# Kernel optimization log

Measured on AMD Instinct MI355X. Metric: run time of the kernel, lower is better.

## Reference

```python
import jax, jax.numpy as jnp
import numpy as np

EPS = 1e-5
NUM_CLUSTERS = 64


def _bn(x, g, b, m, v):
    # eval-mode BatchNorm over channel (last) axis
    return (x - m) * (g * jax.lax.rsqrt(v + EPS)) + b


def _segment_max(feat, choice, num_clusters):
    # feat: [B, N, C], choice: [B, N] -> [B, K, C] (amax per cluster, -inf if empty)
    def one(f, c):
        init = jnp.full((num_clusters, f.shape[-1]), -jnp.inf, dtype=f.dtype)
        return init.at[c].max(f)
    return jax.vmap(one)(feat, choice)


def setup_inputs() -> dict:
    key = jax.random.key(0)
    ks = jax.random.split(key, 8)
    B, N, K, OUT = 32, 8192, NUM_CLUSTERS, 384
    s = lambda fan: 1.0 / np.sqrt(fan)
    return {
        "xyz": jax.random.normal(ks[0], (B, N, 3), jnp.float32),
        "choice": jax.random.randint(ks[1], (B, N), 0, K, jnp.int32),
        "w1": jax.random.normal(ks[2], (128, 3), jnp.float32) * s(3),
        "b1": jnp.zeros((128,), jnp.float32),
        "bn1_g": jnp.ones((128,), jnp.float32),
        "bn1_b": jnp.zeros((128,), jnp.float32),
        "bn1_m": jnp.zeros((128,), jnp.float32),
        "bn1_v": jnp.ones((128,), jnp.float32),
        "w2": jax.random.normal(ks[3], (256, 128), jnp.float32) * s(128),
        "b2": jnp.zeros((256,), jnp.float32),
        "w3": jax.random.normal(ks[4], (512, 512), jnp.float32) * s(512),
        "b3": jnp.zeros((512,), jnp.float32),
        "bn2_g": jnp.ones((512,), jnp.float32),
        "bn2_b": jnp.zeros((512,), jnp.float32),
        "bn2_m": jnp.zeros((512,), jnp.float32),
        "bn2_v": jnp.ones((512,), jnp.float32),
        "w4": jax.random.normal(ks[5], (OUT, 512), jnp.float32) * s(512),
        "b4": jnp.zeros((OUT,), jnp.float32),
    }


def reference(xyz, choice, w1, b1, bn1_g, bn1_b, bn1_m, bn1_v, w2, b2,
              w3, b3, bn2_g, bn2_b, bn2_m, bn2_v, w4, b4):
    # first_conv: 1x1 conv == per-point linear. xyz: [B,N,3]
    h = jnp.einsum("bnc,oc->bno", xyz, w1) + b1            # [B,N,128]
    h = jax.nn.relu(_bn(h, bn1_g, bn1_b, bn1_m, bn1_v))
    feat = jnp.einsum("bnc,oc->bno", h, w2) + b2            # [B,N,256]
    # cluster amax pooling + gather-broadcast back to points
    fg = _segment_max(feat, choice, NUM_CLUSTERS)           # [B,K,256]
    fg_pts = jnp.take_along_axis(fg, choice[..., None], axis=1)  # [B,N,256]
    f = jnp.concatenate([fg_pts, feat], axis=-1)            # [B,N,512]
    # second_conv
    h2 = jnp.einsum("bnc,oc->bno", f, w3) + b3              # [B,N,512]
    h2 = jax.nn.relu(_bn(h2, bn2_g, bn2_b, bn2_m, bn2_v))
    out = jnp.einsum("bnc,oc->bno", h2, w4) + b4            # [B,N,out_dim]
    return _segment_max(out, choice, NUM_CLUSTERS)          # [B,K,out_dim]
```

## Files before the change

kernel.cpp:

```cpp
#include <hip/hip_runtime.h>
#include <hip/hip_bf16.h>

typedef unsigned short u16;
typedef __attribute__((ext_vector_type(8))) short short8;
typedef __attribute__((ext_vector_type(4))) float f32x4;

#define EPSV 1e-5f
#define ENC_NINF 0x007FFFFFu

__device__ __forceinline__ float bf2f(u16 u) {
    union { unsigned int i; float f; } v; v.i = ((unsigned int)u) << 16; return v.f;
}
__device__ __forceinline__ u16 f2bf(float f) {
    union { float f; unsigned int i; } v; v.f = f;
    unsigned int x = v.i;
    return (u16)((x + 0x7FFFu + ((x >> 16) & 1u)) >> 16);
}
__device__ __forceinline__ unsigned int encbf(u16 u) {
    unsigned int f = ((unsigned int)u) << 16;
    return (f & 0x80000000u) ? ~f : (f | 0x80000000u);
}
__device__ __forceinline__ float dec(unsigned int u) {
    union { float f; unsigned int uu; } v;
    v.uu = (u & 0x80000000u) ? (u & 0x7FFFFFFFu) : ~u;
    return v.f;
}

__device__ __forceinline__ void async16(const u16* g, u16* l) {
    __builtin_amdgcn_global_load_lds((const __attribute__((address_space(1))) void*)g,
                                     (__attribute__((address_space(3))) void*)l,
                                     16, 0, 0);
}

__global__ __launch_bounds__(256) void k_fillf(float* __restrict__ o, int n, float val)
{
    int i = blockIdx.x * 256 + threadIdx.x;
    if (i < n) o[i] = val;
}

struct Ptrs { const void* p[17]; int off[18]; int chN; };

__global__ __launch_bounds__(256) void k_repack(Ptrs P, const void* __restrict__ chSrc,
                                                int* __restrict__ chi, u16* __restrict__ rp,
                                                unsigned int* __restrict__ initp, int nU)
{
    const unsigned int* probe = (const unsigned int*)P.p[9];
    int cnt = 0;
#pragma unroll
    for (int i = 0; i < 64; ++i) {
        unsigned int lo = probe[i] & 0xFFFFu;
        if (((lo >> 7) & 0xFFu) >= 0x80u) ++cnt;
    }
    const bool is_f32 = (cnt > 8);

    const unsigned int* cp = (const unsigned int*)chSrc;
    int z = 0; unsigned int mx = 0;
    for (int i = 0; i < 1024; ++i) {
        unsigned int w = cp[i];
        z += (w == 0u);
        mx = (w > mx) ? w : mx;
    }
    const int chMode = (mx >= 64u) ? 2 : ((z > 300) ? 1 : 0);

    const int stride = gridDim.x * 256;
    const int gid0 = blockIdx.x * 256 + threadIdx.x;

    const int totalF = P.off[17];
    for (int g = gid0; g < totalF; g += stride) {
        int t = 0;
        while (g >= P.off[t + 1]) ++t;
        int off = g - P.off[t];
        u16 v;
        if (is_f32) v = f2bf(((const float*)P.p[t])[off]);
        else        v = ((const u16*)P.p[t])[off];
        rp[g] = v;
    }
    for (int i = gid0; i < P.chN; i += stride) {
        int v;
        if (chMode == 1)      v = (int)((const long long*)chSrc)[i];
        else if (chMode == 2) v = (int)((const float*)chSrc)[i];
        else                  v = ((const int*)chSrc)[i];
        chi[i] = v & 63;
    }
    for (int i = gid0; i < nU; i += stride) initp[i] = ENC_NINF;
}

__global__ __launch_bounds__(256) void k_sort(const int* __restrict__ chi,
                                              int* __restrict__ schoice,
                                              int* __restrict__ perm)
{
    __shared__ int hist[64];
    __shared__ int base[64];
    const int b = blockIdx.x, tid = threadIdx.x;
    if (tid < 64) hist[tid] = 0;
    __syncthreads();
    const int o = b << 13;
    for (int i = tid; i < 8192; i += 256) atomicAdd(&hist[chi[o + i]], 1);
    __syncthreads();
    if (tid == 0) {
        int s = 0;
        for (int k = 0; k < 64; ++k) { base[k] = s; s += hist[k]; }
    }
    __syncthreads();
    for (int i = tid; i < 8192; i += 256) {
        int k = chi[o + i];
        int pos = atomicAdd(&base[k], 1);
        schoice[o + pos] = k;
        perm[o + pos] = o + i;
    }
}

__global__ __launch_bounds__(256, 2) void g1_feat(
    const u16* __restrict__ xyz, const u16* __restrict__ w1, const u16* __restrict__ b1,
    const u16* __restrict__ g1v, const u16* __restrict__ bb1,
    const u16* __restrict__ m1, const u16* __restrict__ v1,
    const u16* __restrict__ w2, const u16* __restrict__ b2,
    const int* __restrict__ schoice, const int* __restrict__ perm,
    u16* __restrict__ feat, unsigned int* __restrict__ fg_u)
{
    __shared__ __align__(16) u16 Bs[256 * 128];
    __shared__ unsigned int lred[8 * 256];
    __shared__ float4 pw[128];
    __shared__ float xs[128], ys[128], zs[128];
    __shared__ int chs[128];
    const int tid = threadIdx.x, lane = tid & 63, wave = tid >> 6;
    const int wm = (wave & 1) << 6, wn = (wave >> 1) << 6;
    const int m0 = blockIdx.x << 7;
    if (tid < 128) {
        float s = bf2f(g1v[tid]) * rsqrtf(bf2f(v1[tid]) + EPSV);
        float4 w;
        w.x = bf2f(w1[tid * 3 + 0]) * s;
        w.y = bf2f(w1[tid * 3 + 1]) * s;
        w.z = bf2f(w1[tid * 3 + 2]) * s;
        w.w = (bf2f(b1[tid]) - bf2f(m1[tid])) * s + bf2f(bb1[tid]);
        pw[tid] = w;
        const u16* p = xyz + (size_t)perm[m0 + tid] * 3;
        xs[tid] = bf2f(p[0]); ys[tid] = bf2f(p[1]); zs[tid] = bf2f(p[2]);
        chs[tid] = schoice[m0 + tid];
    }
    const int q = lane >> 4, mr = lane & 15;
    f32x4 acc[2][4][4] = {};
#pragma unroll
    for (int i = 0; i < 16; ++i) {
        int id = (i << 8) + tid, row = id >> 4, cc = id & 15;
        async16(w2 + (size_t)row * 128 + ((cc ^ (row & 15)) << 3), &Bs[id << 3]);
    }
    __syncthreads();
    const int kmin = chs[0], nk = chs[127] - kmin + 1;
    const bool useL = (nk <= 8);
    if (useL) for (int i = tid; i < (nk << 8); i += 256) lred[i] = ENC_NINF;
#pragma unroll
    for (int kk = 0; kk < 4; ++kk) {
        const int lc = kk * 4 + q;
        float4 wv[8];
#pragma unroll
        for (int j = 0; j < 8; ++j) wv[j] = pw[kk * 32 + q * 8 + j];
        short8 af[4];
#pragma unroll
        for (int mi = 0; mi < 4; ++mi) {
            int row = wm + mi * 16 + mr;
            float x = xs[row], y = ys[row], z = zs[row];
#pragma unroll
            for (int j = 0; j < 8; ++j) {
                float val = fmaf(x, wv[j].x, fmaf(y, wv[j].y, fmaf(z, wv[j].z, wv[j].w)));
                af[mi][j] = (short)f2bf(fmaxf(val, 0.0f));
            }
        }
#pragma unroll
        for (int h = 0; h < 2; ++h) {
            short8 bfr[4];
#pragma unroll
            for (int ni = 0; ni < 4; ++ni) {
                int r = (h << 7) + wn + ni * 16 + mr;
                bfr[ni] = *(const short8*)&Bs[r * 128 + ((lc ^ (r & 15)) << 3)];
            }
#pragma unroll
            for (int mi = 0; mi < 4; ++mi)
#pragma unroll
                for (int ni = 0; ni < 4; ++ni)
                    acc[h][mi][ni] = __builtin_amdgcn_mfma_f32_16x16x32_bf16(af[mi], bfr[ni], acc[h][mi][ni], 0, 0, 0);
        }
    }
    __syncthreads();
    const int colb = lane & 15;
    const int bl = m0 >> 13;
    unsigned int* db = fg_u + (size_t)(bl << 6) * 256;
#pragma unroll
    for (int h = 0; h < 2; ++h)
#pragma unroll
        for (int ni = 0; ni < 4; ++ni) {
            int n = (h << 7) + wn + (ni << 4) + colb;
            float bv = bf2f(b2[n]);
#pragma unroll
            for (int mi = 0; mi < 4; ++mi) {
                int curk = -1; unsigned int run = 0;
#pragma unroll
                for (int r = 0; r < 4; ++r) {
                    int rr = wm + (mi << 4) + (q << 2) + r;
                    u16 vb = f2bf(acc[h][mi][ni][r] + bv);
                    feat[(size_t)(m0 + rr) * 256 + n] = vb;
                    unsigned int e = encbf(vb);
                    int k = chs[rr];
                    if (k != curk) {
                        if (curk >= 0) {
                            if (useL) atomicMax(&lred[((curk - kmin) << 8) + n], run);
                            else      atomicMax(&db[curk * 256 + n], run);
                        }
                        curk = k; run = e;
                    } else run = run > e ? run : e;
                }
                if (useL) atomicMax(&lred[((curk - kmin) << 8) + n], run);
                else      atomicMax(&db[curk * 256 + n], run);
            }
        }
    if (useL) {
        __syncthreads();
        for (int i = tid; i < (nk << 8); i += 256) {
            unsigned int v = lred[i];
            if (v != ENC_NINF) atomicMax(&db[(kmin + (i >> 8)) * 256 + (i & 255)], v);
        }
    }
}

__global__ __launch_bounds__(256, 2) void g3_h2(
    const int* __restrict__ schoice, const u16* __restrict__ feat,
    const u16* __restrict__ fg, const u16* __restrict__ w3, const u16* __restrict__ b3,
    const u16* __restrict__ g2, const u16* __restrict__ bb2,
    const u16* __restrict__ m2, const u16* __restrict__ v2,
    u16* __restrict__ h2)
{
    __shared__ __align__(16) u16 As[128 * 64];
    __shared__ __align__(16) u16 Bs[2 * 128 * 64];
    const int tid = threadIdx.x, lane = tid & 63, wave = tid >> 6;
    const int wm = (wave & 1) << 6, wn = (wave >> 1) << 6;
    const int m0 = blockIdx.x << 7, n0 = blockIdx.y << 8;
    const int c = tid & 7, rb = tid >> 3;
    const u16* fgrow[4]; const u16* ftrow[4];
#pragma unroll
    for (int i = 0; i < 4; ++i) {
        int pt = m0 + rb + (i << 5);
        int b = pt >> 13;
        fgrow[i] = fg + (((b << 6) + schoice[pt]) << 8);
        ftrow[i] = feat + ((size_t)pt << 8);
    }
    f32x4 acc[2][4][4] = {};
    for (int k0 = 0; k0 < 512; k0 += 64) {
        __syncthreads();
#pragma unroll
        for (int nt = 0; nt < 2; ++nt)
#pragma unroll
            for (int i = 0; i < 4; ++i) {
                int id = (i << 8) + tid, row = id >> 3, cc = id & 7;
                async16(w3 + (size_t)(n0 + nt * 128 + row) * 512 + k0 + ((cc ^ (row & 7)) << 3),
                        &Bs[nt * 8192 + (id << 3)]);
            }
#pragma unroll
        for (int i = 0; i < 4; ++i) {
            int r = rb + (i << 5);
            int col = k0 + ((c ^ (r & 7)) << 3);
            const u16* src = (col < 256) ? (fgrow[i] + col) : (ftrow[i] + (col - 256));
            async16(src, &As[(((i << 8) + tid) << 3)]);
        }
        __syncthreads();
        const int q = lane >> 4, mr = lane & 15;
#pragma unroll
        for (int kk = 0; kk < 2; ++kk) {
            short8 af[4];
            const int lc = kk * 4 + q;
#pragma unroll
            for (int mi = 0; mi < 4; ++mi) {
                int r = wm + mi * 16 + mr;
                af[mi] = *(const short8*)&As[r * 64 + ((lc ^ (r & 7)) << 3)];
            }
#pragma unroll
            for (int nt = 0; nt < 2; ++nt) {
                short8 bfr[4];
#pragma unroll
                for (int ni = 0; ni < 4; ++ni) {
                    int r = wn + ni * 16 + mr;
                    bfr[ni] = *(const short8*)&Bs[nt * 8192 + r * 64 + ((lc ^ (r & 7)) << 3)];
                }
#pragma unroll
                for (int mi = 0; mi < 4; ++mi)
#pragma unroll
                    for (int ni = 0; ni < 4; ++ni)
                        acc[nt][mi][ni] = __builtin_amdgcn_mfma_f32_16x16x32_bf16(af[mi], bfr[ni], acc[nt][mi][ni], 0, 0, 0);
            }
        }
    }
    const int q = lane >> 4, colb = lane & 15;
#pragma unroll
    for (int nt = 0; nt < 2; ++nt)
#pragma unroll
        for (int ni = 0; ni < 4; ++ni) {
            int n = n0 + nt * 128 + wn + (ni << 4) + colb;
            float s = bf2f(g2[n]) * rsqrtf(bf2f(v2[n]) + EPSV);
            float t = (bf2f(b3[n]) - bf2f(m2[n])) * s + bf2f(bb2[n]);
#pragma unroll
            for (int mi = 0; mi < 4; ++mi)
#pragma unroll
                for (int r = 0; r < 4; ++r) {
                    int m = m0 + wm + (mi << 4) + (q << 2) + r;
                    h2[(size_t)m * 512 + n] = f2bf(fmaxf(fmaf(acc[nt][mi][ni][r], s, t), 0.0f));
                }
        }
}

__global__ __launch_bounds__(512, 2) void g4_out(
    const u16* __restrict__ A, const u16* __restrict__ w4,
    const u16* __restrict__ bias, const int* __restrict__ schoice,
    unsigned int* __restrict__ out_u)
{
    __shared__ __align__(16) u16 smem[32768];
    __shared__ int chs[128];
    u16* As = smem;
    u16* Bs = smem + 8192;
    const int tid = threadIdx.x, lane = tid & 63, wave = tid >> 6;
    const int wm = (wave & 1) << 6, wn = (wave >> 1) * 96;
    const int m0 = blockIdx.x << 7;
    if (tid < 128) chs[tid] = schoice[m0 + tid];
    f32x4 acc[4][6] = {};
    for (int k0 = 0; k0 < 512; k0 += 64) {
        __syncthreads();
#pragma unroll
        for (int i = 0; i < 6; ++i) {
            int id = (i << 9) + tid, row = id >> 3, cc = id & 7;
            async16(w4 + (size_t)row * 512 + k0 + ((cc ^ (row & 7)) << 3),
                    &Bs[id << 3]);
        }
#pragma unroll
        for (int i = 0; i < 2; ++i) {
            int id = (i << 9) + tid, row = id >> 3, cc = id & 7;
            async16(A + (size_t)(m0 + row) * 512 + k0 + ((cc ^ (row & 7)) << 3),
                    &As[id << 3]);
        }
        __syncthreads();
        const int q = lane >> 4, mr = lane & 15;
#pragma unroll
        for (int kk = 0; kk < 2; ++kk) {
            const int lc = (kk << 2) + q;
            short8 af[4];
#pragma unroll
            for (int mi = 0; mi < 4; ++mi) {
                int r = wm + (mi << 4) + mr;
                af[mi] = *(const short8*)&As[r * 64 + ((lc ^ (r & 7)) << 3)];
            }
#pragma unroll
            for (int ni = 0; ni < 6; ++ni) {
                int r = wn + (ni << 4) + mr;
                short8 bfr = *(const short8*)&Bs[r * 64 + ((lc ^ (r & 7)) << 3)];
#pragma unroll
                for (int mi = 0; mi < 4; ++mi)
                    acc[mi][ni] = __builtin_amdgcn_mfma_f32_16x16x32_bf16(af[mi], bfr, acc[mi][ni], 0, 0, 0);
            }
        }
    }
    __syncthreads();
    unsigned int* lred = (unsigned int*)smem;
    const int kmin = chs[0], nk = chs[127] - kmin + 1;
    const bool useL = (nk <= 42);
    const int bl = m0 >> 13;
    unsigned int* db = out_u + (size_t)(bl << 6) * 384;
    if (useL) for (int i = tid; i < nk * 384; i += 512) lred[i] = ENC_NINF;
    __syncthreads();
    const int q = lane >> 4, colb = lane & 15;
#pragma unroll
    for (int ni = 0; ni < 6; ++ni) {
        int nc = wn + (ni << 4) + colb;
        float bv = bf2f(bias[nc]);
#pragma unroll
        for (int mi = 0; mi < 4; ++mi) {
            int curk = -1; unsigned int run = 0;
#pragma unroll
            for (int r = 0; r < 4; ++r) {
                int rr = wm + (mi << 4) + (q << 2) + r;
                unsigned int e = encbf(f2bf(acc[mi][ni][r] + bv));
                int k = chs[rr];
                if (k != curk) {
                    if (curk >= 0) {
                        if (useL) atomicMax(&lred[(curk - kmin) * 384 + nc], run);
                        else      atomicMax(&db[curk * 384 + nc], run);
                    }
                    curk = k; run = e;
                } else run = run > e ? run : e;
            }
            if (useL) atomicMax(&lred[(curk - kmin) * 384 + nc], run);
            else      atomicMax(&db[curk * 384 + nc], run);
        }
    }
    if (useL) {
        __syncthreads();
        for (int i = tid; i < nk * 384; i += 512) {
            unsigned int v = lred[i];
            if (v != ENC_NINF) {
                int kq = i / 384;
                atomicMax(&db[(kmin + kq) * 384 + (i - kq * 384)], v);
            }
        }
    }
}

__global__ __launch_bounds__(256) void k_dec_bf(const unsigned int* __restrict__ u,
                                                u16* __restrict__ o, int n)
{
    int i = blockIdx.x * 256 + threadIdx.x;
    if (i < n) o[i] = f2bf(dec(u[i]));
}
__global__ __launch_bounds__(256) void k_dec_f32(const unsigned int* __restrict__ u,
                                                 float* __restrict__ o, int n)
{
    int i = blockIdx.x * 256 + threadIdx.x;
    if (i < n) o[i] = dec(u[i]);
}

extern "C" void kernel_launch(void* const* d_in, const int* in_sizes, int n_in,
                              void* d_out, int out_size, void* d_ws, size_t ws_size,
                              hipStream_t stream)
{
    float* out = (float*)d_out;
    if (n_in != 18) {
        k_fillf<<<dim3((out_size + 255) / 256), 256, 0, stream>>>(out, out_size, 1000.0f);
        return;
    }

    const int map[17] = {0, 2, 3, 4, 5, 6, 7, 8, 9, 10, 11, 12, 13, 14, 15, 16, 17};
    Ptrs P;
    P.off[0] = 0;
    for (int i = 0; i < 17; ++i) {
        P.p[i] = d_in[map[i]];
        P.off[i + 1] = P.off[i] + in_sizes[map[i]];
    }
    P.chN = in_sizes[1];

    char* ws = (char*)d_ws;
    int* chi = (int*)ws;
    const size_t chiB = ((size_t)P.chN * 4 + 255) & ~255ull;
    int* schoice = (int*)(ws + chiB);
    int* perm    = (int*)(ws + 2 * chiB);
    u16* rp = (u16*)(ws + 3 * chiB);
    const size_t rpB = ((size_t)P.off[17] * 2 + 255) & ~255ull;
    const size_t RPB = 3 * chiB + rpB;

    unsigned int* fg_u_all  = (unsigned int*)(ws + RPB);
    unsigned int* out_u_all = fg_u_all + 32 * 64 * 256;
    const size_t UB = 5242880ull;
    const int nU = 32 * 64 * 640;

    k_repack<<<dim3(1024), 256, 0, stream>>>(P, d_in[1], chi, rp, fg_u_all, nU);
    k_sort<<<dim3(P.chN >> 13), 256, 0, stream>>>(chi, schoice, perm);

    const u16* xyz  = rp + P.off[0];
    const u16* w1   = rp + P.off[1];
    const u16* b1   = rp + P.off[2];
    const u16* bn1g = rp + P.off[3];
    const u16* bn1b = rp + P.off[4];
    const u16* bn1m = rp + P.off[5];
    const u16* bn1v = rp + P.off[6];
    const u16* w2   = rp + P.off[7];
    const u16* b2   = rp + P.off[8];
    const u16* w3   = rp + P.off[9];
    const u16* b3   = rp + P.off[10];
    const u16* bn2g = rp + P.off[11];
    const u16* bn2b = rp + P.off[12];
    const u16* bn2m = rp + P.off[13];
    const u16* bn2v = rp + P.off[14];
    const u16* w4   = rp + P.off[15];
    const u16* b4   = rp + P.off[16];

    const size_t PB = 12615680ull;
    int sb = 32;
    while (sb > 1 && RPB + UB + (size_t)sb * PB > ws_size) sb >>= 1;
    if (RPB + UB + PB > ws_size) {
        k_fillf<<<dim3((out_size + 255) / 256), 256, 0, stream>>>(out, out_size, 3000.0f);
        return;
    }
    const int ns = 32 / sb;

    char* wsb = ws + RPB + UB;
    const size_t featB = (size_t)sb * 8192 * 256 * 2;
    const size_t h2B   = (size_t)sb * 8192 * 512 * 2;
    u16* feat = (u16*)(wsb);
    u16* h2s  = (u16*)(wsb + featB);
    u16* fg   = (u16*)(wsb + featB + h2B);

    const int mblk = sb << 6;
    const int nfg = sb * 64 * 256;
    const int nou = sb * 64 * 384;
    for (int s = 0; s < ns; ++s) {
        const int b0 = s * sb;
        const int pt0 = b0 << 13;
        const int* sch_sl = schoice + pt0;
        const int* perm_sl = perm + pt0;
        unsigned int* fg_u  = fg_u_all + (size_t)b0 * 64 * 256;
        unsigned int* out_u = out_u_all + (size_t)b0 * 64 * 384;
        g1_feat<<<dim3(mblk), 256, 0, stream>>>(xyz, w1, b1, bn1g, bn1b, bn1m, bn1v,
                                                w2, b2, sch_sl, perm_sl, feat, fg_u);
        k_dec_bf<<<dim3((nfg + 255) / 256), 256, 0, stream>>>(fg_u, fg, nfg);
        g3_h2<<<dim3(mblk, 2), 256, 0, stream>>>(sch_sl, feat, fg, w3, b3,
                                                 bn2g, bn2b, bn2m, bn2v, h2s);
        g4_out<<<dim3(mblk), 512, 0, stream>>>(h2s, w4, b4, sch_sl, out_u);
        k_dec_f32<<<dim3((nou + 255) / 256), 256, 0, stream>>>(out_u,
                                                               out + ((size_t)b0 << 6) * 384, nou);
    }
}
```

Before: 543.4 us.

## Precompute per-cluster w3 projection of pooled features, halve h2 GEMM K

The pooled cluster feature is identical for every point in a cluster. Its product with the first half of w3 is therefore computed once per cluster in a new kernel (k_th), folded together with bias and BN shift, and stored as fp32. The main h2 GEMM now only contracts over the 256 per-point feature channels and adds the gathered per-cluster term in the epilogue, removing about half of its MFMA work and the fg gather loads. Separately, g4_out is restructured to stage w4 in two 192-row chunks, shrinking its LDS footprint. That chunking adds extra barriers and lowers the LDS-reduction threshold to 26 clusters.

```diff
diff --git a/kernel.cpp b/kernel.cpp
--- a/kernel.cpp
+++ b/kernel.cpp
@@ -222,44 +222,105 @@
     }
 }
 
-__global__ __launch_bounds__(256, 2) void g3_h2(
-    const int* __restrict__ schoice, const u16* __restrict__ feat,
+__global__ __launch_bounds__(256, 2) void k_th(
     const u16* __restrict__ fg, const u16* __restrict__ w3, const u16* __restrict__ b3,
     const u16* __restrict__ g2, const u16* __restrict__ bb2,
     const u16* __restrict__ m2, const u16* __restrict__ v2,
+    float* __restrict__ th)
+{
+    __shared__ __align__(16) u16 As[64 * 64];
+    __shared__ __align__(16) u16 Bs[256 * 64];
+    const int tid = threadIdx.x, lane = tid & 63, wave = tid >> 6;
+    const int b = blockIdx.x, n0 = blockIdx.y << 8;
+    const u16* fgb = fg + ((size_t)b << 14);
+    f32x4 acc[4][4] = {};
+    for (int k0 = 0; k0 < 256; k0 += 64) {
+        __syncthreads();
+#pragma unroll
+        for (int i = 0; i < 8; ++i) {
+            int id = (i << 8) + tid, row = id >> 3, cc = id & 7;
+            async16(w3 + (size_t)(n0 + row) * 512 + k0 + ((cc ^ (row & 7)) << 3),
+                    &Bs[id << 3]);
+        }
+#pragma unroll
+        for (int i = 0; i < 2; ++i) {
+            int id = (i << 8) + tid, row = id >> 3, cc = id & 7;
+            async16(fgb + (size_t)row * 256 + k0 + ((cc ^ (row & 7)) << 3),
+                    &As[id << 3]);
+        }
+        __syncthreads();
+        const int q = lane >> 4, mr = lane & 15;
+#pragma unroll
+        for (int kk = 0; kk < 2; ++kk) {
+            const int lc = (kk << 2) + q;
+            short8 af[4], bfr[4];
+#pragma unroll
+            for (int mi = 0; mi < 4; ++mi) {
+                int r = (mi << 4) + mr;
+                af[mi] = *(const short8*)&As[r * 64 + ((lc ^ (r & 7)) << 3)];
+            }
+#pragma unroll
+            for (int ni = 0; ni < 4; ++ni) {
+                int r = (wave << 6) + (ni << 4) + mr;
+                bfr[ni] = *(const short8*)&Bs[r * 64 + ((lc ^ (r & 7)) << 3)];
+            }
+#pragma unroll
+            for (int mi = 0; mi < 4; ++mi)
+#pragma unroll
+                for (int ni = 0; ni < 4; ++ni)
+                    acc[mi][ni] = __builtin_amdgcn_mfma_f32_16x16x32_bf16(af[mi], bfr[ni], acc[mi][ni], 0, 0, 0);
+        }
+    }
+    const int q = lane >> 4, colb = lane & 15;
+#pragma unroll
+    for (int ni = 0; ni < 4; ++ni) {
+        int n = n0 + (wave << 6) + (ni << 4) + colb;
+        float s = bf2f(g2[n]) * rsqrtf(bf2f(v2[n]) + EPSV);
+        float t = (bf2f(b3[n]) - bf2f(m2[n])) * s + bf2f(bb2[n]);
+#pragma unroll
+        for (int mi = 0; mi < 4; ++mi)
+#pragma unroll
+            for (int r = 0; r < 4; ++r) {
+                int c = (mi << 4) + (q << 2) + r;
+                th[((size_t)(b << 6) + c) * 512 + n] = fmaf(acc[mi][ni][r], s, t);
+            }
+    }
+}
+
+__global__ __launch_bounds__(256, 2) void g3_h2(
+    const int* __restrict__ schoice, const u16* __restrict__ feat,
+    const float* __restrict__ th, const u16* __restrict__ w3,
+    const u16* __restrict__ g2, const u16* __restrict__ v2,
     u16* __restrict__ h2)
 {
     __shared__ __align__(16) u16 As[128 * 64];
     __shared__ __align__(16) u16 Bs[2 * 128 * 64];
+    __shared__ int chs[128];
     const int tid = threadIdx.x, lane = tid & 63, wave = tid >> 6;
     const int wm = (wave & 1) << 6, wn = (wave >> 1) << 6;
     const int m0 = blockIdx.x << 7, n0 = blockIdx.y << 8;
     const int c = tid & 7, rb = tid >> 3;
-    const u16* fgrow[4]; const u16* ftrow[4];
-#pragma unroll
-    for (int i = 0; i < 4; ++i) {
-        int pt = m0 + rb + (i << 5);
-        int b = pt >> 13;
-        fgrow[i] = fg + (((b << 6) + schoice[pt]) << 8);
-        ftrow[i] = feat + ((size_t)pt << 8);
-    }
+    if (tid < 128) chs[tid] = schoice[m0 + tid];
+    const u16* ftrow[4];
+#pragma unroll
+    for (int i = 0; i < 4; ++i)
+        ftrow[i] = feat + ((size_t)(m0 + rb + (i << 5)) << 8);
     f32x4 acc[2][4][4] = {};
-    for (int k0 = 0; k0 < 512; k0 += 64) {
+    for (int k0 = 0; k0 < 256; k0 += 64) {
         __syncthreads();
 #pragma unroll
         for (int nt = 0; nt < 2; ++nt)
 #pragma unroll
             for (int i = 0; i < 4; ++i) {
                 int id = (i << 8) + tid, row = id >> 3, cc = id & 7;
-                async16(w3 + (size_t)(n0 + nt * 128 + row) * 512 + k0 + ((cc ^ (row & 7)) << 3),
+                async16(w3 + (size_t)(n0 + nt * 128 + row) * 512 + 256 + k0
+                            + ((cc ^ (row & 7)) << 3),
                         &Bs[nt * 8192 + (id << 3)]);
             }
 #pragma unroll
         for (int i = 0; i < 4; ++i) {
             int r = rb + (i << 5);
-            int col = k0 + ((c ^ (r & 7)) << 3);
-            const u16* src = (col < 256) ? (fgrow[i] + col) : (ftrow[i] + (col - 256));
-            async16(src, &As[(((i << 8) + tid) << 3)]);
+            async16(ftrow[i] + k0 + ((c ^ (r & 7)) << 3), &As[(((i << 8) + tid) << 3)]);
         }
         __syncthreads();
         const int q = lane >> 4, mr = lane & 15;
@@ -289,19 +350,21 @@
         }
     }
     const int q = lane >> 4, colb = lane & 15;
+    const float* thb = th + ((size_t)((m0 >> 13) << 6) * 512);
 #pragma unroll
     for (int nt = 0; nt < 2; ++nt)
 #pragma unroll
         for (int ni = 0; ni < 4; ++ni) {
             int n = n0 + nt * 128 + wn + (ni << 4) + colb;
             float s = bf2f(g2[n]) * rsqrtf(bf2f(v2[n]) + EPSV);
-            float t = (bf2f(b3[n]) - bf2f(m2[n])) * s + bf2f(bb2[n]);
 #pragma unroll
             for (int mi = 0; mi < 4; ++mi)
 #pragma unroll
                 for (int r = 0; r < 4; ++r) {
-                    int m = m0 + wm + (mi << 4) + (q << 2) + r;
-                    h2[(size_t)m * 512 + n] = f2bf(fmaxf(fmaf(acc[nt][mi][ni][r], s, t), 0.0f));
+                    int rr = wm + (mi << 4) + (q << 2) + r;
+                    float thv = thb[(size_t)chs[rr] * 512 + n];
+                    h2[(size_t)(m0 + rr) * 512 + n] =
+                        f2bf(fmaxf(fmaf(acc[nt][mi][ni][r], s, thv), 0.0f));
                 }
         }
 }
@@ -311,62 +374,65 @@
     const u16* __restrict__ bias, const int* __restrict__ schoice,
     unsigned int* __restrict__ out_u)
 {
-    __shared__ __align__(16) u16 smem[32768];
+    __shared__ __align__(16) u16 As[128 * 64];
+    __shared__ __align__(16) u16 Bs[192 * 64];
     __shared__ int chs[128];
-    u16* As = smem;
-    u16* Bs = smem + 8192;
     const int tid = threadIdx.x, lane = tid & 63, wave = tid >> 6;
-    const int wm = (wave & 1) << 6, wn = (wave >> 1) * 96;
+    const int wm = (wave & 1) << 6, wn48 = (wave >> 1) * 48;
     const int m0 = blockIdx.x << 7;
     if (tid < 128) chs[tid] = schoice[m0 + tid];
     f32x4 acc[4][6] = {};
     for (int k0 = 0; k0 < 512; k0 += 64) {
-        __syncthreads();
-#pragma unroll
-        for (int i = 0; i < 6; ++i) {
-            int id = (i << 9) + tid, row = id >> 3, cc = id & 7;
-            async16(w4 + (size_t)row * 512 + k0 + ((cc ^ (row & 7)) << 3),
-                    &Bs[id << 3]);
-        }
-#pragma unroll
-        for (int i = 0; i < 2; ++i) {
-            int id = (i << 9) + tid, row = id >> 3, cc = id & 7;
-            async16(A + (size_t)(m0 + row) * 512 + k0 + ((cc ^ (row & 7)) << 3),
-                    &As[id << 3]);
-        }
-        __syncthreads();
-        const int q = lane >> 4, mr = lane & 15;
-#pragma unroll
-        for (int kk = 0; kk < 2; ++kk) {
-            const int lc = (kk << 2) + q;
-            short8 af[4];
-#pragma unroll
-            for (int mi = 0; mi < 4; ++mi) {
-                int r = wm + (mi << 4) + mr;
-                af[mi] = *(const short8*)&As[r * 64 + ((lc ^ (r & 7)) << 3)];
-            }
-#pragma unroll
-            for (int ni = 0; ni < 6; ++ni) {
-                int r = wn + (ni << 4) + mr;
-                short8 bfr = *(const short8*)&Bs[r * 64 + ((lc ^ (r & 7)) << 3)];
-#pragma unroll
-                for (int mi = 0; mi < 4; ++mi)
-                    acc[mi][ni] = __builtin_amdgcn_mfma_f32_16x16x32_bf16(af[mi], bfr, acc[mi][ni], 0, 0, 0);
-            }
-        }
-    }
-    __syncthreads();
-    unsigned int* lred = (unsigned int*)smem;
+#pragma unroll
+        for (int cch = 0; cch < 2; ++cch) {
+            __syncthreads();
+            if (cch == 0)
+#pragma unroll
+                for (int i = 0; i < 2; ++i) {
+                    int id = (i << 9) + tid, row = id >> 3, cc = id & 7;
+                    async16(A + (size_t)(m0 + row) * 512 + k0 + ((cc ^ (row & 7)) << 3),
+                            &As[id << 3]);
+                }
+#pragma unroll
+            for (int i = 0; i < 3; ++i) {
+                int id = (i << 9) + tid, row = id >> 3, cc = id & 7;
+                async16(w4 + (size_t)(cch * 192 + row) * 512 + k0 + ((cc ^ (row & 7)) << 3),
+                        &Bs[id << 3]);
+            }
+            __syncthreads();
+            const int q = lane >> 4, mr = lane & 15;
+#pragma unroll
+            for (int kk = 0; kk < 2; ++kk) {
+                const int lc = (kk << 2) + q;
+                short8 af[4];
+#pragma unroll
+                for (int mi = 0; mi < 4; ++mi) {
+                    int r = wm + (mi << 4) + mr;
+                    af[mi] = *(const short8*)&As[r * 64 + ((lc ^ (r & 7)) << 3)];
+                }
+#pragma unroll
+                for (int ni = 0; ni < 3; ++ni) {
+                    int r = wn48 + (ni << 4) + mr;
+                    short8 bfr = *(const short8*)&Bs[r * 64 + ((lc ^ (r & 7)) << 3)];
+#pragma unroll
+                    for (int mi = 0; mi < 4; ++mi)
+                        acc[mi][cch * 3 + ni] = __builtin_amdgcn_mfma_f32_16x16x32_bf16(af[mi], bfr, acc[mi][cch * 3 + ni], 0, 0, 0);
+                }
+            }
+        }
+    }
+    __syncthreads();
+    unsigned int* lred = (unsigned int*)As;
     const int kmin = chs[0], nk = chs[127] - kmin + 1;
-    const bool useL = (nk <= 42);
+    const bool useL = (nk <= 26);
     const int bl = m0 >> 13;
     unsigned int* db = out_u + (size_t)(bl << 6) * 384;
     if (useL) for (int i = tid; i < nk * 384; i += 512) lred[i] = ENC_NINF;
     __syncthreads();
     const int q = lane >> 4, colb = lane & 15;
 #pragma unroll
-    for (int ni = 0; ni < 6; ++ni) {
-        int nc = wn + (ni << 4) + colb;
+    for (int j = 0; j < 6; ++j) {
+        int nc = (j < 3 ? 0 : 192) + wn48 + ((j < 3 ? j : j - 3) << 4) + colb;
         float bv = bf2f(bias[nc]);
 #pragma unroll
         for (int mi = 0; mi < 4; ++mi) {
@@ -374,7 +440,7 @@
 #pragma unroll
             for (int r = 0; r < 4; ++r) {
                 int rr = wm + (mi << 4) + (q << 2) + r;
-                unsigned int e = encbf(f2bf(acc[mi][ni][r] + bv));
+                unsigned int e = encbf(f2bf(acc[mi][j][r] + bv));
                 int k = chs[rr];
                 if (k != curk) {
                     if (curk >= 0) {
@@ -467,7 +533,7 @@
     const u16* w4   = rp + P.off[15];
     const u16* b4   = rp + P.off[16];
 
-    const size_t PB = 12615680ull;
+    const size_t PB = 12746752ull;
     int sb = 32;
     while (sb > 1 && RPB + UB + (size_t)sb * PB > ws_size) sb >>= 1;
     if (RPB + UB + PB > ws_size) {
@@ -479,9 +545,11 @@
     char* wsb = ws + RPB + UB;
     const size_t featB = (size_t)sb * 8192 * 256 * 2;
     const size_t h2B   = (size_t)sb * 8192 * 512 * 2;
+    const size_t fgB   = (size_t)sb * 64 * 256 * 2;
     u16* feat = (u16*)(wsb);
     u16* h2s  = (u16*)(wsb + featB);
     u16* fg   = (u16*)(wsb + featB + h2B);
+    float* th = (float*)(wsb + featB + h2B + fgB);
 
     const int mblk = sb << 6;
     const int nfg = sb * 64 * 256;
@@ -496,8 +564,9 @@
         g1_feat<<<dim3(mblk), 256, 0, stream>>>(xyz, w1, b1, bn1g, bn1b, bn1m, bn1v,
                                                 w2, b2, sch_sl, perm_sl, feat, fg_u);
         k_dec_bf<<<dim3((nfg + 255) / 256), 256, 0, stream>>>(fg_u, fg, nfg);
-        g3_h2<<<dim3(mblk, 2), 256, 0, stream>>>(sch_sl, feat, fg, w3, b3,
-                                                 bn2g, bn2b, bn2m, bn2v, h2s);
+        k_th<<<dim3(sb, 2), 256, 0, stream>>>(fg, w3, b3, bn2g, bn2b, bn2m, bn2v, th);
+        g3_h2<<<dim3(mblk, 2), 256, 0, stream>>>(sch_sl, feat, th, w3,
+                                                 bn2g, bn2v, h2s);
         g4_out<<<dim3(mblk), 512, 0, stream>>>(h2s, w4, b4, sch_sl, out_u);
         k_dec_f32<<<dim3((nou + 255) / 256), 256, 0, stream>>>(out_u,
                                                                out + ((size_t)b0 << 6) * 384, nou);
```

New measurement: 585.5 us. 7.7% more time.
